# Performance work log

Hardware: AMD Instinct MI355X
Metric: run time of the kernel (lower is better)

## Reference

```python
import jax, jax.numpy as jnp
import numpy as np

N = 100000        # nodes
E = 1600000       # edges (avg degree 16)
D = 128           # feature dim (in_dim == out_dim)
L = 3             # num_layers
P = 8             # num_parts


def setup_inputs() -> dict:
    key = jax.random.key(0)
    k1, k2, k3, k4, k5, k6 = jax.random.split(key, 6)
    edge_row = jnp.sort(jax.random.randint(k1, (E,), 0, N))
    edge_col = jax.random.randint(k2, (E,), 0, N)
    edge_vals = jax.random.uniform(k3, (E,), dtype=jnp.float32)
    x = jax.random.normal(k4, (N, D), dtype=jnp.float32)
    stacked_params = jax.random.normal(k5, (L, D, D, P), dtype=jnp.float32)
    layer_weights = jax.random.normal(k6, (L, P), dtype=jnp.float32)
    return {"edge_row": edge_row, "edge_col": edge_col, "edge_vals": edge_vals,
            "x": x, "stacked_params": stacked_params, "layer_weights": layer_weights}


def reference(edge_row, edge_col, edge_vals, x, stacked_params, layer_weights):
    n = x.shape[0]
    num_layers = stacked_params.shape[0]
    h = x
    for i in range(num_layers):
        # sparse adj.spmm(h): gather source features, scale by edge value, sum per row
        msg = h[edge_col] * edge_vals[:, None]                       # [E, D]
        ax = jax.ops.segment_sum(msg, edge_row, num_segments=n)      # [N, D]
        # MyLinear: softmax over the num_parts weight, contract parts dim
        w = jax.nn.softmax(layer_weights[i])                         # [P]
        ww = jnp.einsum('oip,p->oi', stacked_params[i], w)           # [D_out, D_in]
        h = ax @ ww.T                                                # [N, D_out]
        if i < num_layers - 1:
            h = jax.nn.relu(h)
    return h
```

## Files before the change

kernel.cpp:

```cpp
#include <hip/hip_runtime.h>
#include <cstdint>

#define D 128
#define P 8
#define L 3

typedef __attribute__((ext_vector_type(8))) _Float16 f16x8;
typedef __attribute__((ext_vector_type(4))) float    f32x4;
typedef __attribute__((ext_vector_type(2))) float    f32x2;
typedef __attribute__((ext_vector_type(4))) uint32_t u32x4;
typedef u32x4 __attribute__((aligned(4))) u32x4_u;

#if __has_builtin(__builtin_amdgcn_cvt_pk_f32_fp8) && __has_builtin(__builtin_amdgcn_cvt_pk_fp8_f32)
#define HAVE_FP8_CVT 1
#else
#define HAVE_FP8_CVT 0
#endif

template<bool HI>
static __device__ __forceinline__ f32x2 fp8_pair(uint32_t u) {
#if HAVE_FP8_CVT
    return __builtin_amdgcn_cvt_pk_f32_fp8((int)u, HI);
#else
    uint32_t w = HI ? (u >> 16) : u;
    f32x2 r;
#pragma unroll
    for (int i = 0; i < 2; i++) {
        uint32_t b = (w >> (8 * i)) & 0xffu;
        uint32_t mag = b & 0x7fu;
        uint16_t h = (uint16_t)(((b & 0x80u) << 8) | ((mag >= 8u) ? ((mag << 7) + 0x2000u) : 0u));
        union { uint16_t q; _Float16 hf; } c; c.q = h;
        r[i] = (float)c.hf;
    }
    return r;
#endif
}

static __device__ __forceinline__ uint32_t f32_to_fp8(float v) {
#if HAVE_FP8_CVT
    return (uint32_t)__builtin_amdgcn_cvt_pk_fp8_f32(v, v, 0, false) & 0xffu;
#else
    union { _Float16 hf; uint16_t q; } c; c.hf = (_Float16)v;
    uint32_t s = ((uint32_t)c.q >> 8) & 0x80u;
    int t = (int)(c.q & 0x7fff) - 0x2000;
    if (t < 0) return s;
    int r = (t + 63 + ((t >> 7) & 1)) >> 7;
    if (r > 0x7e) r = 0x7e;
    return s | (uint32_t)r;
#endif
}

__global__ void prep_all(const int* __restrict__ er, const int* __restrict__ col,
                         const float* __restrict__ vals,
                         const float* __restrict__ sp, const float* __restrict__ lw,
                         int* __restrict__ rp, uint32_t* __restrict__ epk,
                         _Float16* __restrict__ wwB, int n, int e) {
    int i = blockIdx.x * blockDim.x + threadIdx.x;
    if (i < e) {
        union { _Float16 h; uint16_t u; } v;
        v.h = (_Float16)vals[i];
        epk[i] = ((uint32_t)col[i] << 15) | (uint32_t)(v.u & 0x7FFFu);
        int cur = er[i];
        if (i == 0) {
            for (int r = 0; r <= cur; r++) rp[r] = 0;
        } else {
            int prev = er[i - 1];
            for (int r = prev + 1; r <= cur; r++) rp[r] = i;
        }
        if (i == e - 1) {
            for (int r = cur + 1; r <= n; r++) rp[r] = e;
        }
    }
    if (i < L * D * D) {
        int l = i / (D * D);
        int rem = i - l * D * D;
        int o = rem / D;
        int ii = rem - o * D;
        float wv[P];
        float m = -1e30f;
#pragma unroll
        for (int p = 0; p < P; p++) { wv[p] = lw[l * P + p]; m = fmaxf(m, wv[p]); }
        float s = 0.f;
#pragma unroll
        for (int p = 0; p < P; p++) { wv[p] = __expf(wv[p] - m); s += wv[p]; }
        float inv = 1.0f / s;
        const float* spp = sp + ((size_t)(l * D + o) * D + ii) * P;
        float acc = 0.f;
#pragma unroll
        for (int p = 0; p < P; p++) acc += spp[p] * wv[p];
        int kt = ii >> 5, kp = ii & 31;
        wwB[(((l * 4 + kt) * D + o) << 5) + kp] = (_Float16)(acc * inv);
    }
}

static __device__ __forceinline__ void mfma2w_q8(const _Float16 (*s_h)[136],
                                                 const _Float16* __restrict__ wwB_l,
                                                 uint8_t* __restrict__ y8,
                                                 float* __restrict__ scl,
                                                 unsigned* srow,
                                                 int row0, int n, int tid) {
    const int w = tid >> 6, lane = tid & 63;
    const int quad = lane >> 4, l16 = lane & 15;
    f32x4 acc[4] = {};
#pragma unroll
    for (int kt = 0; kt < 4; kt++) {
        f16x8 af = *(const f16x8*)&s_h[l16][kt * 32 + quad * 8];
#pragma unroll
        for (int c = 0; c < 4; c++) {
            const int ct = w * 4 + c;
            f16x8 bf = *(const f16x8*)&wwB_l[((kt * D + ct * 16 + l16) << 5) + quad * 8];
            acc[c] = __builtin_amdgcn_mfma_f32_16x16x32_f16(af, bf, acc[c], 0, 0, 0);
        }
    }
#pragma unroll
    for (int rg = 0; rg < 4; rg++) {
        float m = fmaxf(fmaxf(fabsf(acc[0][rg]), fabsf(acc[1][rg])),
                        fmaxf(fabsf(acc[2][rg]), fabsf(acc[3][rg])));
#pragma unroll
        for (int d = 1; d < 16; d <<= 1) m = fmaxf(m, __shfl_xor(m, d));
        if (l16 == 0) atomicMax(&srow[quad * 4 + rg], __float_as_uint(m));
    }
    __syncthreads();
#pragma unroll
    for (int rg = 0; rg < 4; rg++) {
        const int rr = quad * 4 + rg;
        const int row = row0 + rr;
        float rmax = fmaxf(__uint_as_float(srow[rr]), 1e-20f);
        float qs = 448.f / rmax;
        if (row < n) {
#pragma unroll
            for (int c = 0; c < 4; c++) {
                const int ct = w * 4 + c;
                float v = acc[c][rg] * qs;
                v = fminf(fmaxf(v, -448.f), 448.f);
                y8[row * D + ct * 16 + l16] = (uint8_t)f32_to_fp8(v);
            }
            if (w == 0 && l16 == 0) scl[row] = rmax * (1.f / 448.f);
        }
    }
}

__global__ __launch_bounds__(128, 8)
void gemm_x32(const float* __restrict__ x, const _Float16* __restrict__ wwB_l,
              uint8_t* __restrict__ y8, float* __restrict__ scl, int n) {
    __shared__ _Float16 s_h[16][136];
    __shared__ unsigned srow[16];
    const int tid = threadIdx.x;
    const int row0 = blockIdx.x * 16;
    const int sg = tid >> 4;
    const int c8 = (tid & 15) * 8;
    if (tid < 16) srow[tid] = 0;
#pragma unroll
    for (int h2 = 0; h2 < 2; h2++) {
        int rr = sg + h2 * 8;
        int row = row0 + rr;
        float4 v0 = {}, v1 = {};
        if (row < n) {
            v0 = *(const float4*)&x[row * D + c8];
            v1 = *(const float4*)&x[row * D + c8 + 4];
        }
        f16x8 h;
        h[0] = (_Float16)v0.x; h[1] = (_Float16)v0.y;
        h[2] = (_Float16)v0.z; h[3] = (_Float16)v0.w;
        h[4] = (_Float16)v1.x; h[5] = (_Float16)v1.y;
        h[6] = (_Float16)v1.z; h[7] = (_Float16)v1.w;
        *(f16x8*)&s_h[rr][c8] = h;
    }
    __syncthreads();
    mfma2w_q8(s_h, wwB_l, y8, scl, srow, row0, n, tid);
}

template<int NB>
static __device__ __forceinline__ void gather_chunk8(float (&a)[8],
                                                     const uint8_t* __restrict__ y8,
                                                     const uint32_t* __restrict__ epk,
                                                     const float* __restrict__ scl,
                                                     int e, int c8) {
    uint32_t m[NB];
#pragma unroll
    for (int j = 0; j < NB; j++) m[j] = epk[e + j];
    uint2 g[NB]; float sc[NB];
#pragma unroll
    for (int j = 0; j < NB; j++) {
        uint32_t row = m[j] >> 15;
        g[j]  = *(const uint2*)&y8[row * (uint32_t)D + (uint32_t)c8];
        sc[j] = scl[row];
    }
#pragma unroll
    for (int j = 0; j < NB; j++) {
        union { uint16_t u; _Float16 h; } vv; vv.u = (uint16_t)(m[j] & 0x7FFFu);
        float vf = (float)vv.h * sc[j];
        f32x2 p;
        p = fp8_pair<false>(g[j].x); a[0] += vf * p[0]; a[1] += vf * p[1];
        p = fp8_pair<true >(g[j].x); a[2] += vf * p[0]; a[3] += vf * p[1];
        p = fp8_pair<false>(g[j].y); a[4] += vf * p[0]; a[5] += vf * p[1];
        p = fp8_pair<true >(g[j].y); a[6] += vf * p[0]; a[7] += vf * p[1];
    }
}

static __device__ __forceinline__ void gather_row8_pipe(float (&a)[8],
                                                        const uint8_t* __restrict__ y8,
                                                        const uint32_t* __restrict__ epk,
                                                        const float* __restrict__ scl,
                                                        int e, int e1, int c8) {
    const int nfull = (e1 - e) >> 3;
    u32x4 mA = {}, mB = {};
    if (nfull > 0) {
        mA = *(const u32x4_u*)&epk[e];
        mB = *(const u32x4_u*)&epk[e + 4];
    }
    for (int c = 0; c < nfull; c++) {
        uint32_t m[8] = { mA.x, mA.y, mA.z, mA.w, mB.x, mB.y, mB.z, mB.w };
        uint2 g[8]; float sc[8];
#pragma unroll
        for (int j = 0; j < 8; j++) {
            uint32_t row = m[j] >> 15;
            g[j]  = *(const uint2*)&y8[row * (uint32_t)D + (uint32_t)c8];
            sc[j] = scl[row];
        }
        if (c + 1 < nfull) {
            const int en = e + (c + 1) * 8;
            mA = *(const u32x4_u*)&epk[en];
            mB = *(const u32x4_u*)&epk[en + 4];
        }
#pragma unroll
        for (int j = 0; j < 8; j++) {
            union { uint16_t u; _Float16 h; } vv; vv.u = (uint16_t)(m[j] & 0x7FFFu);
            float vf = (float)vv.h * sc[j];
            f32x2 p;
            p = fp8_pair<false>(g[j].x); a[0] += vf * p[0]; a[1] += vf * p[1];
            p = fp8_pair<true >(g[j].x); a[2] += vf * p[0]; a[3] += vf * p[1];
            p = fp8_pair<false>(g[j].y); a[4] += vf * p[0]; a[5] += vf * p[1];
            p = fp8_pair<true >(g[j].y); a[6] += vf * p[0]; a[7] += vf * p[1];
        }
    }
    e += nfull * 8;
    if (e + 4 <= e1) { gather_chunk8<4>(a, y8, epk, scl, e, c8); e += 4; }
    for (; e < e1; e++) gather_chunk8<1>(a, y8, epk, scl, e, c8);
}

__global__ __launch_bounds__(128, 8)
void fused_layer(const uint8_t* __restrict__ yprev, const float* __restrict__ sprev,
                 const int* __restrict__ rp, const uint32_t* __restrict__ epk,
                 const _Float16* __restrict__ wwB_l,
                 uint8_t* __restrict__ ynext, float* __restrict__ snext, int n) {
    __shared__ _Float16 s_h[16][136];
    __shared__ unsigned srow[16];
    const int tid = threadIdx.x;
    const int row0 = blockIdx.x * 16;
    const int sg = tid >> 4;
    const int c8 = (tid & 15) * 8;
    if (tid < 16) srow[tid] = 0;
#pragma unroll
    for (int h2 = 0; h2 < 2; h2++) {
        const int rr = sg + h2 * 8;
        const int r = row0 + rr;
        float a[8] = {0.f, 0.f, 0.f, 0.f, 0.f, 0.f, 0.f, 0.f};
        if (r < n) gather_row8_pipe(a, yprev, epk, sprev, rp[r], rp[r + 1], c8);
        f16x8 o;
#pragma unroll
        for (int k = 0; k < 8; k++) o[k] = (_Float16)fmaxf(a[k], 0.f);
        *(f16x8*)&s_h[rr][c8] = o;
    }
    __syncthreads();
    mfma2w_q8(s_h, wwB_l, ynext, snext, srow, row0, n, tid);
}

__global__ __launch_bounds__(128, 8)
void spmm_f32(const uint8_t* __restrict__ y8, const float* __restrict__ sprev,
              const int* __restrict__ rp, const uint32_t* __restrict__ epk,
              float* __restrict__ out, int n) {
    const int tid = threadIdx.x;
    const int r = blockIdx.x * 8 + (tid >> 4);
    const int c8 = (tid & 15) * 8;
    if (r >= n) return;
    float a[8] = {0.f, 0.f, 0.f, 0.f, 0.f, 0.f, 0.f, 0.f};
    gather_row8_pipe(a, y8, epk, sprev, rp[r], rp[r + 1], c8);
    *(float4*)&out[(size_t)r * D + c8]     = make_float4(a[0], a[1], a[2], a[3]);
    *(float4*)&out[(size_t)r * D + c8 + 4] = make_float4(a[4], a[5], a[6], a[7]);
}

extern "C" void kernel_launch(void* const* d_in, const int* in_sizes, int n_in,
                              void* d_out, int out_size, void* d_ws, size_t ws_size,
                              hipStream_t stream) {
    const int*   edge_row  = (const int*)d_in[0];
    const int*   edge_col  = (const int*)d_in[1];
    const float* edge_vals = (const float*)d_in[2];
    const float* x         = (const float*)d_in[3];
    const float* sp        = (const float*)d_in[4];
    const float* lw        = (const float*)d_in[5];
    float* out = (float*)d_out;

    const int E_ = in_sizes[0];
    const int N_ = in_sizes[3] / D;

    char* ws = (char*)d_ws;
    int* row_ptr = (int*)ws;
    size_t off = (((size_t)(N_ + 1) * sizeof(int)) + 255) & ~(size_t)255;
    uint32_t* epk = (uint32_t*)(ws + off);
    off += (size_t)E_ * sizeof(uint32_t);
    off = (off + 255) & ~(size_t)255;
    _Float16* wwB = (_Float16*)(ws + off);
    off += (size_t)L * 4 * D * 32 * sizeof(_Float16);
    off = (off + 255) & ~(size_t)255;
    uint8_t* y8A = (uint8_t*)(ws + off);
    off += (size_t)N_ * D;
    uint8_t* y8B = (uint8_t*)(ws + off);
    off += (size_t)N_ * D;
    off = (off + 255) & ~(size_t)255;
    float* scA = (float*)(ws + off);
    off += (size_t)N_ * sizeof(float);
    float* scB = (float*)(ws + off);

    const int pgrid = (E_ > L * D * D ? E_ : L * D * D);
    prep_all<<<(pgrid + 255) / 256, 256, 0, stream>>>(edge_row, edge_col, edge_vals,
                                                      sp, lw, row_ptr, epk, wwB, N_, E_);

    const int sblk = (N_ + 15) / 16;
    const int WWL = 4 * D * 32;

    gemm_x32<<<sblk, 128, 0, stream>>>(x, wwB, y8A, scA, N_);
    fused_layer<<<sblk, 128, 0, stream>>>(y8A, scA, row_ptr, epk, wwB + WWL,     y8B, scB, N_);
    fused_layer<<<sblk, 128, 0, stream>>>(y8B, scB, row_ptr, epk, wwB + 2 * WWL, y8A, scA, N_);
    spmm_f32<<<(N_ + 7) / 8, 128, 0, stream>>>(y8A, scA, row_ptr, epk, out, N_);
}
```

Measured before the change: 270.9 us.

## Split gather into XCD-aware column slices and decouple from dense GEMM

```diff
diff --git a/kernel.cpp b/kernel.cpp
--- a/kernel.cpp
+++ b/kernel.cpp
@@ -8,8 +8,6 @@
 typedef __attribute__((ext_vector_type(8))) _Float16 f16x8;
 typedef __attribute__((ext_vector_type(4))) float    f32x4;
 typedef __attribute__((ext_vector_type(2))) float    f32x2;
-typedef __attribute__((ext_vector_type(4))) uint32_t u32x4;
-typedef u32x4 __attribute__((aligned(4))) u32x4_u;
 
 #if __has_builtin(__builtin_amdgcn_cvt_pk_f32_fp8) && __has_builtin(__builtin_amdgcn_cvt_pk_fp8_f32)
 #define HAVE_FP8_CVT 1
@@ -171,19 +169,17 @@
 }
 
 template<int NB>
-static __device__ __forceinline__ void gather_chunk8(float (&a)[8],
-                                                     const uint8_t* __restrict__ y8,
-                                                     const uint32_t* __restrict__ epk,
-                                                     const float* __restrict__ scl,
-                                                     int e, int c8) {
+static __device__ __forceinline__ void gslice_chunk(float (&a)[4],
+        const uint8_t* __restrict__ y8, const uint32_t* __restrict__ epk,
+        const float* __restrict__ scl, int e, int cb) {
     uint32_t m[NB];
 #pragma unroll
-    for (int j = 0; j < NB; j++) m[j] = epk[e + j];
-    uint2 g[NB]; float sc[NB];
+    for (int j = 0; j < NB; j++) m[j] = __builtin_nontemporal_load(&epk[e + j]);
+    uint32_t g[NB]; float sc[NB];
 #pragma unroll
     for (int j = 0; j < NB; j++) {
         uint32_t row = m[j] >> 15;
-        g[j]  = *(const uint2*)&y8[row * (uint32_t)D + (uint32_t)c8];
+        g[j]  = *(const uint32_t*)&y8[row * (uint32_t)D + (uint32_t)cb];
         sc[j] = scl[row];
     }
 #pragma unroll
@@ -191,93 +187,93 @@
         union { uint16_t u; _Float16 h; } vv; vv.u = (uint16_t)(m[j] & 0x7FFFu);
         float vf = (float)vv.h * sc[j];
         f32x2 p;
-        p = fp8_pair<false>(g[j].x); a[0] += vf * p[0]; a[1] += vf * p[1];
-        p = fp8_pair<true >(g[j].x); a[2] += vf * p[0]; a[3] += vf * p[1];
-        p = fp8_pair<false>(g[j].y); a[4] += vf * p[0]; a[5] += vf * p[1];
-        p = fp8_pair<true >(g[j].y); a[6] += vf * p[0]; a[7] += vf * p[1];
-    }
-}
-
-static __device__ __forceinline__ void gather_row8_pipe(float (&a)[8],
-                                                        const uint8_t* __restrict__ y8,
-                                                        const uint32_t* __restrict__ epk,
-                                                        const float* __restrict__ scl,
-                                                        int e, int e1, int c8) {
-    const int nfull = (e1 - e) >> 3;
-    u32x4 mA = {}, mB = {};
-    if (nfull > 0) {
-        mA = *(const u32x4_u*)&epk[e];
-        mB = *(const u32x4_u*)&epk[e + 4];
-    }
-    for (int c = 0; c < nfull; c++) {
-        uint32_t m[8] = { mA.x, mA.y, mA.z, mA.w, mB.x, mB.y, mB.z, mB.w };
-        uint2 g[8]; float sc[8];
-#pragma unroll
-        for (int j = 0; j < 8; j++) {
-            uint32_t row = m[j] >> 15;
-            g[j]  = *(const uint2*)&y8[row * (uint32_t)D + (uint32_t)c8];
-            sc[j] = scl[row];
-        }
-        if (c + 1 < nfull) {
-            const int en = e + (c + 1) * 8;
-            mA = *(const u32x4_u*)&epk[en];
-            mB = *(const u32x4_u*)&epk[en + 4];
-        }
-#pragma unroll
-        for (int j = 0; j < 8; j++) {
-            union { uint16_t u; _Float16 h; } vv; vv.u = (uint16_t)(m[j] & 0x7FFFu);
-            float vf = (float)vv.h * sc[j];
-            f32x2 p;
-            p = fp8_pair<false>(g[j].x); a[0] += vf * p[0]; a[1] += vf * p[1];
-            p = fp8_pair<true >(g[j].x); a[2] += vf * p[0]; a[3] += vf * p[1];
-            p = fp8_pair<false>(g[j].y); a[4] += vf * p[0]; a[5] += vf * p[1];
-            p = fp8_pair<true >(g[j].y); a[6] += vf * p[0]; a[7] += vf * p[1];
-        }
-    }
-    e += nfull * 8;
-    if (e + 4 <= e1) { gather_chunk8<4>(a, y8, epk, scl, e, c8); e += 4; }
-    for (; e < e1; e++) gather_chunk8<1>(a, y8, epk, scl, e, c8);
+        p = fp8_pair<false>(g[j]); a[0] += vf * p[0]; a[1] += vf * p[1];
+        p = fp8_pair<true >(g[j]); a[2] += vf * p[0]; a[3] += vf * p[1];
+    }
+}
+
+static __device__ __forceinline__ void gslice_row(float (&a)[4],
+        const uint8_t* __restrict__ y8, const uint32_t* __restrict__ epk,
+        const float* __restrict__ scl, int e, int e1, int cb) {
+    for (; e + 8 <= e1; e += 8) gslice_chunk<8>(a, y8, epk, scl, e, cb);
+    if (e + 4 <= e1) { gslice_chunk<4>(a, y8, epk, scl, e, cb); e += 4; }
+    for (; e < e1; e++) gslice_chunk<1>(a, y8, epk, scl, e, cb);
 }
 
 __global__ __launch_bounds__(128, 8)
-void fused_layer(const uint8_t* __restrict__ yprev, const float* __restrict__ sprev,
-                 const int* __restrict__ rp, const uint32_t* __restrict__ epk,
-                 const _Float16* __restrict__ wwB_l,
-                 uint8_t* __restrict__ ynext, float* __restrict__ snext, int n) {
+void gather_ax(const uint8_t* __restrict__ y8, const float* __restrict__ scl,
+               const int* __restrict__ rp, const uint32_t* __restrict__ epk,
+               _Float16* __restrict__ ax, int rbeg, int rend, int nrb) {
+    const int bid = blockIdx.x;
+    const int xcd = bid & 7;
+    const int slice = xcd >> 1;
+    const int rb = (bid >> 3) * 2 + (xcd & 1);
+    if (rb >= nrb) return;
+    const int tid = threadIdx.x;
+    const int sg = tid >> 3, l8 = tid & 7;
+    const int cb = slice * 32 + l8 * 4;
+    const int r0 = rbeg + rb * 32 + sg * 2;
+#pragma unroll 1
+    for (int q = 0; q < 2; q++) {
+        const int r = r0 + q;
+        if (r >= rend) continue;
+        float a[4] = {0.f, 0.f, 0.f, 0.f};
+        gslice_row(a, y8, epk, scl, rp[r], rp[r + 1], cb);
+        union { _Float16 h[4]; unsigned long long u; } o;
+#pragma unroll
+        for (int k = 0; k < 4; k++) o.h[k] = (_Float16)fmaxf(a[k], 0.f);
+        __builtin_nontemporal_store(o.u,
+            (unsigned long long*)&ax[(size_t)(r - rbeg) * D + cb]);
+    }
+}
+
+__global__ __launch_bounds__(128, 8)
+void gather_out(const uint8_t* __restrict__ y8, const float* __restrict__ scl,
+                const int* __restrict__ rp, const uint32_t* __restrict__ epk,
+                float* __restrict__ out, int n, int nrb) {
+    const int bid = blockIdx.x;
+    const int xcd = bid & 7;
+    const int slice = xcd >> 1;
+    const int rb = (bid >> 3) * 2 + (xcd & 1);
+    if (rb >= nrb) return;
+    const int tid = threadIdx.x;
+    const int sg = tid >> 3, l8 = tid & 7;
+    const int cb = slice * 32 + l8 * 4;
+    const int r0 = rb * 32 + sg * 2;
+#pragma unroll 1
+    for (int q = 0; q < 2; q++) {
+        const int r = r0 + q;
+        if (r >= n) continue;
+        float a[4] = {0.f, 0.f, 0.f, 0.f};
+        gslice_row(a, y8, epk, scl, rp[r], rp[r + 1], cb);
+        unsigned long long* op = (unsigned long long*)&out[(size_t)r * D + cb];
+        union { float f[2]; unsigned long long u; } w;
+        w.f[0] = a[0]; w.f[1] = a[1]; __builtin_nontemporal_store(w.u, op);
+        w.f[0] = a[2]; w.f[1] = a[3]; __builtin_nontemporal_store(w.u, op + 1);
+    }
+}
+
+__global__ __launch_bounds__(128, 8)
+void dense_q8(const _Float16* __restrict__ ax, const _Float16* __restrict__ wwB_l,
+              uint8_t* __restrict__ y8o, float* __restrict__ sclo,
+              int rbeg, int rend) {
     __shared__ _Float16 s_h[16][136];
     __shared__ unsigned srow[16];
     const int tid = threadIdx.x;
-    const int row0 = blockIdx.x * 16;
+    const int row0 = rbeg + blockIdx.x * 16;
     const int sg = tid >> 4;
     const int c8 = (tid & 15) * 8;
     if (tid < 16) srow[tid] = 0;
 #pragma unroll
     for (int h2 = 0; h2 < 2; h2++) {
-        const int rr = sg + h2 * 8;
-        const int r = row0 + rr;
-        float a[8] = {0.f, 0.f, 0.f, 0.f, 0.f, 0.f, 0.f, 0.f};
-        if (r < n) gather_row8_pipe(a, yprev, epk, sprev, rp[r], rp[r + 1], c8);
-        f16x8 o;
-#pragma unroll
-        for (int k = 0; k < 8; k++) o[k] = (_Float16)fmaxf(a[k], 0.f);
-        *(f16x8*)&s_h[rr][c8] = o;
+        int rr = sg + h2 * 8;
+        int row = row0 + rr;
+        f16x8 h = {0, 0, 0, 0, 0, 0, 0, 0};
+        if (row < rend) h = *(const f16x8*)&ax[(size_t)(row - rbeg) * D + c8];
+        *(f16x8*)&s_h[rr][c8] = h;
     }
     __syncthreads();
-    mfma2w_q8(s_h, wwB_l, ynext, snext, srow, row0, n, tid);
-}
-
-__global__ __launch_bounds__(128, 8)
-void spmm_f32(const uint8_t* __restrict__ y8, const float* __restrict__ sprev,
-              const int* __restrict__ rp, const uint32_t* __restrict__ epk,
-              float* __restrict__ out, int n) {
-    const int tid = threadIdx.x;
-    const int r = blockIdx.x * 8 + (tid >> 4);
-    const int c8 = (tid & 15) * 8;
-    if (r >= n) return;
-    float a[8] = {0.f, 0.f, 0.f, 0.f, 0.f, 0.f, 0.f, 0.f};
-    gather_row8_pipe(a, y8, epk, sprev, rp[r], rp[r + 1], c8);
-    *(float4*)&out[(size_t)r * D + c8]     = make_float4(a[0], a[1], a[2], a[3]);
-    *(float4*)&out[(size_t)r * D + c8 + 4] = make_float4(a[4], a[5], a[6], a[7]);
+    mfma2w_q8(s_h, wwB_l, y8o, sclo, srow, row0, rend, tid);
 }
 
 extern "C" void kernel_launch(void* const* d_in, const int* in_sizes, int n_in,
@@ -311,16 +307,41 @@
     float* scA = (float*)(ws + off);
     off += (size_t)N_ * sizeof(float);
     float* scB = (float*)(ws + off);
+    off += (size_t)N_ * sizeof(float);
+    off = (off + 255) & ~(size_t)255;
+    _Float16* axb = (_Float16*)(ws + off);
 
     const int pgrid = (E_ > L * D * D ? E_ : L * D * D);
     prep_all<<<(pgrid + 255) / 256, 256, 0, stream>>>(edge_row, edge_col, edge_vals,
                                                       sp, lw, row_ptr, epk, wwB, N_, E_);
 
-    const int sblk = (N_ + 15) / 16;
     const int WWL = 4 * D * 32;
-
-    gemm_x32<<<sblk, 128, 0, stream>>>(x, wwB, y8A, scA, N_);
-    fused_layer<<<sblk, 128, 0, stream>>>(y8A, scA, row_ptr, epk, wwB + WWL,     y8B, scB, N_);
-    fused_layer<<<sblk, 128, 0, stream>>>(y8B, scB, row_ptr, epk, wwB + 2 * WWL, y8A, scA, N_);
-    spmm_f32<<<(N_ + 7) / 8, 128, 0, stream>>>(y8A, scA, row_ptr, epk, out, N_);
-}
+    const int Nh0 = ((N_ + 63) / 64) * 32;
+    const int Nh = Nh0 < N_ ? Nh0 : N_;
+
+    gemm_x32<<<(N_ + 15) / 16, 128, 0, stream>>>(x, wwB, y8A, scA, N_);
+
+    struct Seg { int b, e; };
+    Seg segs[2] = { {0, Nh}, {Nh, N_} };
+    const uint8_t* yin[2] = { y8A, y8B };
+    const float*   sin[2] = { scA, scB };
+    uint8_t* yout[2] = { y8B, y8A };
+    float*   sout[2] = { scB, scA };
+    for (int l = 0; l < 2; l++) {
+        for (int h = 0; h < 2; h++) {
+            const int rb0 = segs[h].b, rb1 = segs[h].e;
+            const int nrows = rb1 - rb0;
+            if (nrows <= 0) continue;
+            const int nrb = (nrows + 31) / 32;
+            const int grid = ((nrb + 1) / 2) * 8;
+            gather_ax<<<grid, 128, 0, stream>>>(yin[l], sin[l], row_ptr, epk,
+                                                axb, rb0, rb1, nrb);
+            dense_q8<<<(nrows + 15) / 16, 128, 0, stream>>>(axb, wwB + (l + 1) * WWL,
+                                                            yout[l], sout[l], rb0, rb1);
+        }
+    }
+
+    const int nrbF = (N_ + 31) / 32;
+    const int gridF = ((nrbF + 1) / 2) * 8;
+    gather_out<<<gridF, 128, 0, stream>>>(y8A, scA, row_ptr, epk, out, N_, nrbF);
+}
```

New measurement: 586.8 us. +116.6%, slower.
